# Optimization experiments

Measured on AMD Instinct MI355X. Metric: run time of the kernel, lower is better.

The kernel has to match this reference:

```python
import jax, jax.numpy as jnp
import numpy as np

N = 50000
E = 800000
EPS = 1e-5


def setup_inputs() -> dict:
    key = jax.random.key(0)
    ks = jax.random.split(key, 12)

    def w(k, fi, fo):
        return jax.random.normal(k, (fi, fo), dtype=jnp.float32) * (1.0 / np.sqrt(fi))

    return {
        "x": jax.random.normal(ks[0], (N, 128), dtype=jnp.float32),
        "edge_index": jax.random.randint(ks[1], (2, E), 0, N, dtype=jnp.int32),
        "W1": w(ks[2], 128, 256), "b1": jnp.zeros((256,), jnp.float32),
        "g1": jnp.ones((256,), jnp.float32), "be1": jnp.zeros((256,), jnp.float32),
        "W2": w(ks[3], 256, 128), "b2": jnp.zeros((128,), jnp.float32),
        "g2": jnp.ones((128,), jnp.float32), "be2": jnp.zeros((128,), jnp.float32),
        "W3": w(ks[4], 128, 64), "b3": jnp.zeros((64,), jnp.float32),
        "g3": jnp.ones((64,), jnp.float32), "be3": jnp.zeros((64,), jnp.float32),
        "W4": w(ks[5], 64, 40), "b4": jnp.zeros((40,), jnp.float32),
        "a": jnp.array(0.25, dtype=jnp.float32),  # PReLU single shared weight
    }


def _gcn_norm(edge_index, n):
    # PyG GCNConv default: add self-loops, symmetric normalization.
    loop = jnp.arange(n, dtype=edge_index.dtype)
    s = jnp.concatenate([edge_index[0], loop])  # [E+N] source nodes
    d = jnp.concatenate([edge_index[1], loop])  # [E+N] dest nodes
    deg = jax.ops.segment_sum(jnp.ones_like(s, dtype=jnp.float32), d, num_segments=n)
    dinv = jax.lax.rsqrt(jnp.maximum(deg, 1.0))  # deg >= 1 due to self-loops
    norm = dinv[s] * dinv[d]                     # [E+N]
    return s, d, norm


def _gcn_conv(x, W, b, s, d, norm, n):
    xw = x @ W                                   # [N, F_out] dense transform
    msg = xw[s] * norm[:, None]                  # gather + edge scaling
    return jax.ops.segment_sum(msg, d, num_segments=n) + b  # scatter-add


def _bn(x, g, b):
    # BatchNorm over nodes (training statistics, biased variance)
    m = jnp.mean(x, axis=0)
    v = jnp.var(x, axis=0)
    return (x - m) * jax.lax.rsqrt(v + EPS) * g + b


def _prelu(x, a):
    return jnp.where(x >= 0, x, a * x)


def reference(x, edge_index, W1, b1, g1, be1, W2, b2, g2, be2,
              W3, b3, g3, be3, W4, b4, a):
    n = x.shape[0]
    s, d, norm = _gcn_norm(edge_index, n)
    h = _prelu(_bn(_gcn_conv(x, W1, b1, s, d, norm, n), g1, be1), a)
    h = _prelu(_bn(_gcn_conv(h, W2, b2, s, d, norm, n), g2, be2), a)
    h = _prelu(_bn(_gcn_conv(h, W3, b3, s, d, norm, n), g3, be3), a)
    h = _gcn_conv(h, W4, b4, s, d, norm, n)
    return jax.nn.log_softmax(h, axis=1)
```

## Files before the change

kernel.cpp:

```cpp
#include <hip/hip_runtime.h>
#include <cstdint>
#include <cmath>

typedef _Float16 half_t;
typedef _Float16 h2 __attribute__((ext_vector_type(2)));
typedef _Float16 h8 __attribute__((ext_vector_type(8)));
typedef float f4 __attribute__((ext_vector_type(4)));


__global__ __launch_bounds__(256) void csr_hist_kernel(const int* __restrict__ ei_dst,
                                                       int* __restrict__ hcnt,
                                                       int E, int B, int NB, int chunk) {
    __shared__ int hist[256];
    int t = threadIdx.x;
    hist[t] = 0;
    __syncthreads();
    int base = blockIdx.x * chunk;
    int lim = min(base + chunk, E);
    for (int e = base + t; e < lim; e += 256) {
        int dst = ei_dst[e];
        atomicAdd(&hist[dst >> 8], 1);
    }
    __syncthreads();
    if (t < B) hcnt[t * NB + blockIdx.x] = hist[t];
}

__global__ __launch_bounds__(256) void csr_bscan_kernel(int* __restrict__ hcnt,
                                                        int* __restrict__ btot, int NB) {
    __shared__ int sh[256];
    int b = blockIdx.x, t = threadIdx.x;
    int v = (t < NB) ? hcnt[b * NB + t] : 0;
    sh[t] = v;
    __syncthreads();
    for (int off = 1; off < 256; off <<= 1) {
        int u = (t >= off) ? sh[t - off] : 0;
        __syncthreads();
        sh[t] += u;
        __syncthreads();
    }
    if (t < NB) hcnt[b * NB + t] = sh[t] - v;
    if (t == 255) btot[b] = sh[255];
}

__global__ __launch_bounds__(256) void csr_ebase_kernel(const int* __restrict__ btot,
                                                        int* __restrict__ edge_base,
                                                        int* __restrict__ row_ptr,
                                                        int B, int E, int n) {
    __shared__ int sh[256];
    int t = threadIdx.x;
    int v = (t < B) ? btot[t] : 0;
    sh[t] = v;
    __syncthreads();
    for (int off = 1; off < 256; off <<= 1) {
        int u = (t >= off) ? sh[t - off] : 0;
        __syncthreads();
        sh[t] += u;
        __syncthreads();
    }
    if (t < B) edge_base[t] = sh[t] - v;
    if (t == 0) {
        edge_base[B] = E;
        row_ptr[n] = E;
    }
}

__global__ __launch_bounds__(256) void csr_part_kernel(const int* __restrict__ ei,
                                                       const int* __restrict__ hcnt,
                                                       const int* __restrict__ edge_base,
                                                       unsigned int* __restrict__ ebuf,
                                                       int E, int B, int NB, int chunk) {
    __shared__ int lcur[256];
    int t = threadIdx.x;
    if (t < B) lcur[t] = edge_base[t] + hcnt[t * NB + blockIdx.x];
    __syncthreads();
    int base = blockIdx.x * chunk;
    int lim = min(base + chunk, E);
    for (int e = base + t; e < lim; e += 256) {
        int src = ei[e];
        int dst = ei[E + e];
        int b = dst >> 8;
        int pos = atomicAdd(&lcur[b], 1);
        ebuf[pos] = ((unsigned int)(dst & 255) << 16) | (unsigned int)src;
    }
}

__global__ __launch_bounds__(256) void csr_fill_kernel(const unsigned int* __restrict__ ebuf,
                                                       const int* __restrict__ edge_base,
                                                       int* __restrict__ row_ptr,
                                                       float* __restrict__ dinv,
                                                       unsigned short* __restrict__ colidx,
                                                       int n) {
    __shared__ int cnt[256];
    __shared__ int sc[256];
    __shared__ int cur[256];
    int b = blockIdx.x;
    int t = threadIdx.x;
    int seg_beg = edge_base[b];
    int seg_end = edge_base[b + 1];
    cnt[t] = 0;
    __syncthreads();
    for (int e = seg_beg + t; e < seg_end; e += 256)
        atomicAdd(&cnt[ebuf[e] >> 16], 1);
    __syncthreads();
    sc[t] = cnt[t];
    __syncthreads();
    for (int off = 1; off < 256; off <<= 1) {
        int u = (t >= off) ? sc[t - off] : 0;
        __syncthreads();
        sc[t] += u;
        __syncthreads();
    }
    int excl = seg_beg + sc[t] - cnt[t];
    int node = (b << 8) + t;
    if (node < n) {
        row_ptr[node] = excl;
        dinv[node] = rsqrtf((float)cnt[t] + 1.0f);
    }
    cur[t] = excl;
    __syncthreads();
    for (int e = seg_beg + t; e < seg_end; e += 256) {
        unsigned int p = ebuf[e];
        int pos = atomicAdd(&cur[p >> 16], 1);
        colidx[pos] = (unsigned short)(p & 0xffff);
    }
}


__global__ void f2h_kernel(const float* __restrict__ x, half_t* __restrict__ xh, int total4) {
    int i = blockIdx.x * blockDim.x + threadIdx.x;
    if (i < total4) {
        float4 v = *(const float4*)&x[i * 4];
        half_t* p = xh + (size_t)i * 4;
        p[0] = (half_t)v.x; p[1] = (half_t)v.y; p[2] = (half_t)v.z; p[3] = (half_t)v.w;
    }
}

__global__ __launch_bounds__(256) void wtall_kernel(const float* __restrict__ W1,
                                                    const float* __restrict__ W2,
                                                    const float* __restrict__ W3,
                                                    const float* __restrict__ W4,
                                                    half_t* __restrict__ W1t,
                                                    half_t* __restrict__ W2t,
                                                    half_t* __restrict__ W3t,
                                                    half_t* __restrict__ W4t) {
    int idx = blockIdx.x * blockDim.x + threadIdx.x;
    if (idx < 32768) {
        int n = idx >> 7, k = idx & 127;
        W1t[idx] = (half_t)W1[k * 256 + n];
    } else if (idx < 65536) {
        int r = idx - 32768;
        int n = r >> 8, k = r & 255;
        W2t[r] = (half_t)W2[k * 128 + n];
    } else if (idx < 73728) {
        int r = idx - 65536;
        int n = r >> 7, k = r & 127;
        W3t[r] = (half_t)W3[k * 64 + n];
    } else if (idx < 77824) {
        int r = idx - 73728;
        int n = r >> 6, k = r & 63;
        W4t[r] = (n < 40) ? (half_t)W4[k * 40 + n] : (half_t)0.f;
    }
}


__global__ __launch_bounds__(256) void aggh128_kernel(const half_t* __restrict__ in,
                                                      half_t* __restrict__ out,
                                                      const int* __restrict__ row_ptr,
                                                      const unsigned short* __restrict__ colidx,
                                                      const float* __restrict__ dinv, int n) {
    int node = blockIdx.x * 4 + (threadIdx.x >> 6);
    if (node >= n) return;
    int c = threadIdx.x & 63;
    float dv = dinv[node];
    h2 self = *(const h2*)(in + (size_t)node * 128 + 2 * c);
    float acc0 = dv * (float)self[0], acc1 = dv * (float)self[1];
    int beg = row_ptr[node], end = row_ptr[node + 1];
    for (int k = beg; k < end; k += 8) {
        int idx[8]; float w[8]; h2 v[8];
#pragma unroll
        for (int j = 0; j < 8; ++j) idx[j] = colidx[k + j];
#pragma unroll
        for (int j = 0; j < 8; ++j) w[j] = (k + j < end) ? dinv[idx[j]] : 0.f;
#pragma unroll
        for (int j = 0; j < 8; ++j) v[j] = *(const h2*)(in + (size_t)idx[j] * 128 + 2 * c);
#pragma unroll
        for (int j = 0; j < 8; ++j) {
            acc0 = fmaf(w[j], (float)v[j][0], acc0);
            acc1 = fmaf(w[j], (float)v[j][1], acc1);
        }
    }
    h2 r;
    r[0] = (half_t)(dv * acc0);
    r[1] = (half_t)(dv * acc1);
    *(h2*)(out + (size_t)node * 128 + 2 * c) = r;
}

__global__ __launch_bounds__(256) void aggh64_kernel(const half_t* __restrict__ in,
                                                     half_t* __restrict__ out,
                                                     const int* __restrict__ row_ptr,
                                                     const unsigned short* __restrict__ colidx,
                                                     const float* __restrict__ dinv, int n) {
    int node = blockIdx.x * 4 + (threadIdx.x >> 6);
    if (node >= n) return;
    int c = threadIdx.x & 63;
    float dv = dinv[node];
    float acc = dv * (float)in[(size_t)node * 64 + c];
    int beg = row_ptr[node], end = row_ptr[node + 1];
    for (int k = beg; k < end; k += 8) {
        int idx[8]; float w[8]; float v[8];
#pragma unroll
        for (int j = 0; j < 8; ++j) idx[j] = colidx[k + j];
#pragma unroll
        for (int j = 0; j < 8; ++j) w[j] = (k + j < end) ? dinv[idx[j]] : 0.f;
#pragma unroll
        for (int j = 0; j < 8; ++j) v[j] = (float)in[(size_t)idx[j] * 64 + c];
#pragma unroll
        for (int j = 0; j < 8; ++j) acc = fmaf(w[j], v[j], acc);
    }
    out[(size_t)node * 64 + c] = (half_t)(dv * acc);
}

__global__ __launch_bounds__(256) void aggsm64_kernel(const half_t* __restrict__ in,
                                                      float* __restrict__ out,
                                                      const int* __restrict__ row_ptr,
                                                      const unsigned short* __restrict__ colidx,
                                                      const float* __restrict__ dinv,
                                                      const float* __restrict__ b4, int n) {
    int node = blockIdx.x * 4 + (threadIdx.x >> 6);
    if (node >= n) return;
    int c = threadIdx.x & 31;
    float dv = dinv[node];
    h2 self = *(const h2*)(in + (size_t)node * 64 + 2 * c);
    float acc0 = dv * (float)self[0], acc1 = dv * (float)self[1];
    int beg = row_ptr[node], end = row_ptr[node + 1];
    for (int k = beg; k < end; k += 8) {
        int idx[8]; float w[8]; h2 v[8];
#pragma unroll
        for (int j = 0; j < 8; ++j) idx[j] = colidx[k + j];
#pragma unroll
        for (int j = 0; j < 8; ++j) w[j] = (k + j < end) ? dinv[idx[j]] : 0.f;
#pragma unroll
        for (int j = 0; j < 8; ++j) v[j] = *(const h2*)(in + (size_t)idx[j] * 64 + 2 * c);
#pragma unroll
        for (int j = 0; j < 8; ++j) {
            acc0 = fmaf(w[j], (float)v[j][0], acc0);
            acc1 = fmaf(w[j], (float)v[j][1], acc1);
        }
    }
    int col0 = 2 * c, col1 = 2 * c + 1;
    float z0 = (col0 < 40) ? (dv * acc0 + b4[col0]) : -INFINITY;
    float z1 = (col1 < 40) ? (dv * acc1 + b4[col1]) : -INFINITY;
    float m = fmaxf(z0, z1);
#pragma unroll
    for (int off = 16; off > 0; off >>= 1) m = fmaxf(m, __shfl_xor(m, off, 64));
    float e0 = (col0 < 40) ? expf(z0 - m) : 0.f;
    float e1 = (col1 < 40) ? expf(z1 - m) : 0.f;
    float s = e0 + e1;
#pragma unroll
    for (int off = 16; off > 0; off >>= 1) s += __shfl_xor(s, off, 64);
    float ls = logf(s);
    if (c < 20) {
        float2 r = make_float2(z0 - m - ls, z1 - m - ls);
        *(float2*)(out + (size_t)node * 40 + 2 * c) = r;
    }
}


template <int K, int NT, bool FUSE>
__global__ __launch_bounds__(256) void mgemm_kernel(const half_t* __restrict__ A,
                                                    const half_t* __restrict__ Wt,
                                                    const float* __restrict__ AB,
                                                    const float* __restrict__ pa,
                                                    half_t* __restrict__ C,
                                                    int M, int Nc, int nTiles) {
    constexpr int NR = NT * 16;
    constexpr int CH = K / 8;
    constexpr int LOG_CH = (CH == 8) ? 3 : (CH == 16 ? 4 : 5);
    __shared__ half_t wlds[NR * K];

    for (int idx = threadIdx.x; idx < NR * CH; idx += 256) {
        int row = idx >> LOG_CH;
        int c = idx & (CH - 1);
        *(h8*)(wlds + ((size_t)c * NR + row) * 8) = *(const h8*)(Wt + (size_t)idx * 8);
    }
    int wave = threadIdx.x >> 6;
    int lane = threadIdx.x & 63;
    int l16 = lane & 15, kgrp = lane >> 4;
    float alpha = FUSE ? pa[0] : 0.f;
    __syncthreads();

    for (int tile = blockIdx.x; tile < nTiles; tile += gridDim.x) {
        int r0 = tile * 64 + wave * 16;
        int arow = r0 + l16;
        bool rowok = (arow < M);
        const half_t* Ap = A + (size_t)arow * K + kgrp * 8;
        h8 af[K / 32];
#pragma unroll
        for (int kk = 0; kk < K / 32; ++kk) {
            h8 v;
            if (rowok) {
                v = *(const h8*)(Ap + kk * 32);
            } else {
#pragma unroll
                for (int j = 0; j < 8; ++j) v[j] = (half_t)0.f;
            }
            if (FUSE) {
                int kb = kk * 32 + kgrp * 8;
#pragma unroll
                for (int j = 0; j < 8; ++j) {
                    float u = (float)v[j] * AB[kb + j] + AB[256 + kb + j];
                    u = (u >= 0.f) ? u : alpha * u;
                    v[j] = (half_t)u;
                }
            }
            af[kk] = v;
        }

        for (int nt = 0; nt < NT; ++nt) {
            f4 acc = {0.f, 0.f, 0.f, 0.f};
#pragma unroll
            for (int kk = 0; kk < K / 32; ++kk) {
                h8 bf = *(const h8*)(wlds + ((size_t)(kk * 4 + kgrp) * NR + nt * 16 + l16) * 8);
                acc = __builtin_amdgcn_mfma_f32_16x16x32_f16(af[kk], bf, acc, 0, 0, 0);
            }
            int col = nt * 16 + l16;
            if (col < Nc) {
#pragma unroll
                for (int j = 0; j < 4; ++j) {
                    int row = r0 + kgrp * 4 + j;
                    if (row < M) C[(size_t)row * Nc + col] = (half_t)acc[j];
                }
            }
        }
    }
}


template <int F>
__global__ __launch_bounds__(256) void stats2_kernel(const half_t* __restrict__ z,
                                                     float* __restrict__ sums, int n) {
    constexpr int CB = F / 8;
    constexpr int RG = 256 / CB;
    __shared__ float red[256][16];
    int t = threadIdx.x;
    int cb = t % CB;
    int rg = t / CB;
    float sm[8], sq[8];
#pragma unroll
    for (int j = 0; j < 8; ++j) { sm[j] = 0.f; sq[j] = 0.f; }
    for (int r = blockIdx.x * RG + rg; r < n; r += gridDim.x * RG) {
        h8 v = *(const h8*)(z + (size_t)r * F + cb * 8);
#pragma unroll
        for (int j = 0; j < 8; ++j) {
            float f = (float)v[j];
            sm[j] += f;
            sq[j] = fmaf(f, f, sq[j]);
        }
    }
#pragma unroll
    for (int j = 0; j < 8; ++j) { red[t][j] = sm[j]; red[t][8 + j] = sq[j]; }
    __syncthreads();
    for (int o = t; o < 2 * F; o += 256) {
        int c = o % F, kind = o / F;
        int cbo = c >> 3, ci = (c & 7) + kind * 8;
        float v = 0.f;
#pragma unroll
        for (int g = 0; g < RG; ++g) v += red[g * CB + cbo][ci];
        atomicAdd(&sums[kind * 256 + c], v);
    }
}

__global__ void bnfin_kernel(const float* __restrict__ sums, const float* __restrict__ g,
                             const float* __restrict__ be, float* __restrict__ AB, int n, int F) {
    int c = threadIdx.x;
    if (c >= F) return;
    float mean = sums[c] / (float)n;
    float var = sums[256 + c] / (float)n - mean * mean;
    float rstd = rsqrtf(var + 1e-5f);
    float sc = g[c] * rstd;
    AB[c] = sc;
    AB[256 + c] = be[c] - mean * sc;
}


extern "C" void kernel_launch(void* const* d_in, const int* in_sizes, int n_in,
                              void* d_out, int out_size, void* d_ws, size_t ws_size,
                              hipStream_t stream) {
    const float* x   = (const float*)d_in[0];
    const int*   ei  = (const int*)d_in[1];
    const float* W1  = (const float*)d_in[2];
    const float* g1  = (const float*)d_in[4];
    const float* be1 = (const float*)d_in[5];
    const float* W2  = (const float*)d_in[6];
    const float* g2  = (const float*)d_in[8];
    const float* be2 = (const float*)d_in[9];
    const float* W3  = (const float*)d_in[10];
    const float* g3  = (const float*)d_in[12];
    const float* be3 = (const float*)d_in[13];
    const float* W4  = (const float*)d_in[14];
    const float* b4  = (const float*)d_in[15];
    const float* pa  = (const float*)d_in[16];

    int N = in_sizes[0] / 128;
    int E = in_sizes[1] / 2;
    int B = (N + 255) >> 8;
    int chunk = (((E + 255) / 256) + 255) & ~255;
    int NB = (E + chunk - 1) / chunk;

    char* ws = (char*)d_ws;
    size_t off = 0;
    auto carve = [&](size_t bytes) -> char* {
        char* p = ws + off;
        off += (bytes + 255) & ~(size_t)255;
        return p;
    };
    float*          dinv      = (float*)carve((size_t)N * 4);
    int*            row_ptr   = (int*)carve((size_t)(N + 1) * 4);
    int*            hcnt      = (int*)carve((size_t)B * NB * 4);
    int*            btot      = (int*)carve((size_t)B * 4);
    int*            edge_base = (int*)carve((size_t)(B + 1) * 4);
    unsigned int*   ebuf      = (unsigned int*)carve((size_t)E * 4);
    unsigned short* colidx    = (unsigned short*)carve((size_t)(E + 16) * 2);
    float*          stats     = (float*)carve(3 * 512 * 4);
    float*          bnAB      = (float*)carve(512 * 4);
    half_t* W1t = (half_t*)carve((size_t)256 * 128 * 2);
    half_t* W2t = (half_t*)carve((size_t)128 * 256 * 2);
    half_t* W3t = (half_t*)carve((size_t)64 * 128 * 2);
    half_t* W4t = (half_t*)carve((size_t)64 * 64 * 2);
    half_t* hA  = (half_t*)carve((size_t)N * 256 * 2);
    half_t* hB  = (half_t*)carve((size_t)N * 128 * 2);
    half_t* hC  = (half_t*)carve((size_t)N * 128 * 2);
    half_t* hD1 = (half_t*)carve((size_t)N * 64 * 2);
    half_t* hD2 = (half_t*)carve((size_t)N * 64 * 2);
    half_t* hE  = (half_t*)carve((size_t)N * 64 * 2);
    (void)n_in; (void)out_size; (void)ws_size;

    hipMemsetAsync(colidx + E, 0, 32, stream);
    hipMemsetAsync(stats, 0, 3 * 512 * 4, stream);

    csr_hist_kernel<<<NB, 256, 0, stream>>>(ei + E, hcnt, E, B, NB, chunk);
    csr_bscan_kernel<<<B, 256, 0, stream>>>(hcnt, btot, NB);
    csr_ebase_kernel<<<1, 256, 0, stream>>>(btot, edge_base, row_ptr, B, E, N);
    csr_part_kernel<<<NB, 256, 0, stream>>>(ei, hcnt, edge_base, ebuf, E, B, NB, chunk);
    csr_fill_kernel<<<B, 256, 0, stream>>>(ebuf, edge_base, row_ptr, dinv, colidx, N);

    wtall_kernel<<<(77824 + 255) / 256, 256, 0, stream>>>(W1, W2, W3, W4, W1t, W2t, W3t, W4t);

    int nTiles = (N + 63) / 64;
    int gb = nTiles < 512 ? nTiles : 512;
    int ab = (N + 3) / 4;

    f2h_kernel<<<(N * 128 / 4 + 255) / 256, 256, 0, stream>>>(x, hB, N * 128 / 4);
    aggh128_kernel<<<ab, 256, 0, stream>>>(hB, hC, row_ptr, colidx, dinv, N);
    mgemm_kernel<128, 16, false><<<gb, 256, 0, stream>>>(hC, W1t, nullptr, nullptr, hA,
                                                         N, 256, nTiles);
    stats2_kernel<256><<<512, 256, 0, stream>>>(hA, stats, N);
    bnfin_kernel<<<1, 256, 0, stream>>>(stats, g1, be1, bnAB, N, 256);

    mgemm_kernel<256, 8, true><<<gb, 256, 0, stream>>>(hA, W2t, bnAB, pa, hB, N, 128, nTiles);
    aggh128_kernel<<<ab, 256, 0, stream>>>(hB, hC, row_ptr, colidx, dinv, N);
    stats2_kernel<128><<<512, 256, 0, stream>>>(hC, stats + 512, N);
    bnfin_kernel<<<1, 256, 0, stream>>>(stats + 512, g2, be2, bnAB, N, 128);

    mgemm_kernel<128, 4, true><<<gb, 256, 0, stream>>>(hC, W3t, bnAB, pa, hD1, N, 64, nTiles);
    aggh64_kernel<<<ab, 256, 0, stream>>>(hD1, hD2, row_ptr, colidx, dinv, N);
    stats2_kernel<64><<<512, 256, 0, stream>>>(hD2, stats + 1024, N);
    bnfin_kernel<<<1, 256, 0, stream>>>(stats + 1024, g3, be3, bnAB, N, 64);

    mgemm_kernel<64, 4, true><<<gb, 256, 0, stream>>>(hD2, W4t, bnAB, pa, hE, N, 64, nTiles);
    aggsm64_kernel<<<ab, 256, 0, stream>>>(hE, (float*)d_out, row_ptr, colidx, dinv, b4, N);
}
```

Before: 298.2 us.

## Fuse BatchNorm statistics into GEMM/aggregation epilogues and drop conversion kernels

BatchNorm sum and sum-of-squares accumulation moves into the epilogues of the GEMM and aggregation kernels, using shared-memory atomics followed by global atomics. The BN scale/offset finalize is recomputed in each consuming GEMM's prologue. The first-layer aggregation now reads fp32 input directly, removing the separate f2h conversion pass. The two memsets are merged into one. This removes six kernel launches and the extra full-tensor reads done by stats2, at the cost of more shared-memory atomic contention in the aggregation and GEMM kernels.

```diff
diff --git a/kernel.cpp b/kernel.cpp
--- a/kernel.cpp
+++ b/kernel.cpp
@@ -125,15 +125,6 @@
     }
 }
 
-
-__global__ void f2h_kernel(const float* __restrict__ x, half_t* __restrict__ xh, int total4) {
-    int i = blockIdx.x * blockDim.x + threadIdx.x;
-    if (i < total4) {
-        float4 v = *(const float4*)&x[i * 4];
-        half_t* p = xh + (size_t)i * 4;
-        p[0] = (half_t)v.x; p[1] = (half_t)v.y; p[2] = (half_t)v.z; p[3] = (half_t)v.w;
-    }
-}
 
 __global__ __launch_bounds__(256) void wtall_kernel(const float* __restrict__ W1,
                                                     const float* __restrict__ W2,
@@ -163,7 +154,7 @@
 }
 
 
-__global__ __launch_bounds__(256) void aggh128_kernel(const half_t* __restrict__ in,
+__global__ __launch_bounds__(256) void agg128f_kernel(const float* __restrict__ in,
                                                       half_t* __restrict__ out,
                                                       const int* __restrict__ row_ptr,
                                                       const unsigned short* __restrict__ colidx,
@@ -172,21 +163,21 @@
     if (node >= n) return;
     int c = threadIdx.x & 63;
     float dv = dinv[node];
-    h2 self = *(const h2*)(in + (size_t)node * 128 + 2 * c);
-    float acc0 = dv * (float)self[0], acc1 = dv * (float)self[1];
+    float2 self = *(const float2*)(in + (size_t)node * 128 + 2 * c);
+    float acc0 = dv * self.x, acc1 = dv * self.y;
     int beg = row_ptr[node], end = row_ptr[node + 1];
     for (int k = beg; k < end; k += 8) {
-        int idx[8]; float w[8]; h2 v[8];
+        int idx[8]; float w[8]; float2 v[8];
 #pragma unroll
         for (int j = 0; j < 8; ++j) idx[j] = colidx[k + j];
 #pragma unroll
         for (int j = 0; j < 8; ++j) w[j] = (k + j < end) ? dinv[idx[j]] : 0.f;
 #pragma unroll
-        for (int j = 0; j < 8; ++j) v[j] = *(const h2*)(in + (size_t)idx[j] * 128 + 2 * c);
+        for (int j = 0; j < 8; ++j) v[j] = *(const float2*)(in + (size_t)idx[j] * 128 + 2 * c);
 #pragma unroll
         for (int j = 0; j < 8; ++j) {
-            acc0 = fmaf(w[j], (float)v[j][0], acc0);
-            acc1 = fmaf(w[j], (float)v[j][1], acc1);
+            acc0 = fmaf(w[j], v[j].x, acc0);
+            acc1 = fmaf(w[j], v[j].y, acc1);
         }
     }
     h2 r;
@@ -195,29 +186,110 @@
     *(h2*)(out + (size_t)node * 128 + 2 * c) = r;
 }
 
+template <bool STATS>
+__global__ __launch_bounds__(256) void aggh128_kernel(const half_t* __restrict__ in,
+                                                      half_t* __restrict__ out,
+                                                      const int* __restrict__ row_ptr,
+                                                      const unsigned short* __restrict__ colidx,
+                                                      const float* __restrict__ dinv,
+                                                      float* __restrict__ sout, int n) {
+    __shared__ float ssum[128], ssq[128];
+    int t = threadIdx.x;
+    if (STATS) {
+        if (t < 128) { ssum[t] = 0.f; ssq[t] = 0.f; }
+        __syncthreads();
+    }
+    int node = blockIdx.x * 4 + (t >> 6);
+    bool active = node < n;
+    int c = t & 63;
+    float dv = 0.f, acc0 = 0.f, acc1 = 0.f;
+    if (active) {
+        dv = dinv[node];
+        h2 self = *(const h2*)(in + (size_t)node * 128 + 2 * c);
+        acc0 = dv * (float)self[0];
+        acc1 = dv * (float)self[1];
+        int beg = row_ptr[node], end = row_ptr[node + 1];
+        for (int k = beg; k < end; k += 8) {
+            int idx[8]; float w[8]; h2 v[8];
+#pragma unroll
+            for (int j = 0; j < 8; ++j) idx[j] = colidx[k + j];
+#pragma unroll
+            for (int j = 0; j < 8; ++j) w[j] = (k + j < end) ? dinv[idx[j]] : 0.f;
+#pragma unroll
+            for (int j = 0; j < 8; ++j) v[j] = *(const h2*)(in + (size_t)idx[j] * 128 + 2 * c);
+#pragma unroll
+            for (int j = 0; j < 8; ++j) {
+                acc0 = fmaf(w[j], (float)v[j][0], acc0);
+                acc1 = fmaf(w[j], (float)v[j][1], acc1);
+            }
+        }
+        float v0 = dv * acc0, v1 = dv * acc1;
+        h2 r;
+        r[0] = (half_t)v0;
+        r[1] = (half_t)v1;
+        *(h2*)(out + (size_t)node * 128 + 2 * c) = r;
+        if (STATS) {
+            atomicAdd(&ssum[2 * c], v0);
+            atomicAdd(&ssq[2 * c], v0 * v0);
+            atomicAdd(&ssum[2 * c + 1], v1);
+            atomicAdd(&ssq[2 * c + 1], v1 * v1);
+        }
+    }
+    if (STATS) {
+        __syncthreads();
+        if (t < 128) {
+            atomicAdd(&sout[t], ssum[t]);
+            atomicAdd(&sout[256 + t], ssq[t]);
+        }
+    }
+}
+
+template <bool STATS>
 __global__ __launch_bounds__(256) void aggh64_kernel(const half_t* __restrict__ in,
                                                      half_t* __restrict__ out,
                                                      const int* __restrict__ row_ptr,
                                                      const unsigned short* __restrict__ colidx,
-                                                     const float* __restrict__ dinv, int n) {
-    int node = blockIdx.x * 4 + (threadIdx.x >> 6);
-    if (node >= n) return;
-    int c = threadIdx.x & 63;
-    float dv = dinv[node];
-    float acc = dv * (float)in[(size_t)node * 64 + c];
-    int beg = row_ptr[node], end = row_ptr[node + 1];
-    for (int k = beg; k < end; k += 8) {
-        int idx[8]; float w[8]; float v[8];
-#pragma unroll
-        for (int j = 0; j < 8; ++j) idx[j] = colidx[k + j];
-#pragma unroll
-        for (int j = 0; j < 8; ++j) w[j] = (k + j < end) ? dinv[idx[j]] : 0.f;
-#pragma unroll
-        for (int j = 0; j < 8; ++j) v[j] = (float)in[(size_t)idx[j] * 64 + c];
-#pragma unroll
-        for (int j = 0; j < 8; ++j) acc = fmaf(w[j], v[j], acc);
-    }
-    out[(size_t)node * 64 + c] = (half_t)(dv * acc);
+                                                     const float* __restrict__ dinv,
+                                                     float* __restrict__ sout, int n) {
+    __shared__ float ssum[64], ssq[64];
+    int t = threadIdx.x;
+    if (STATS) {
+        if (t < 64) { ssum[t] = 0.f; ssq[t] = 0.f; }
+        __syncthreads();
+    }
+    int node = blockIdx.x * 4 + (t >> 6);
+    bool active = node < n;
+    int c = t & 63;
+    float dv = 0.f, acc = 0.f;
+    if (active) {
+        dv = dinv[node];
+        acc = dv * (float)in[(size_t)node * 64 + c];
+        int beg = row_ptr[node], end = row_ptr[node + 1];
+        for (int k = beg; k < end; k += 8) {
+            int idx[8]; float w[8]; float v[8];
+#pragma unroll
+            for (int j = 0; j < 8; ++j) idx[j] = colidx[k + j];
+#pragma unroll
+            for (int j = 0; j < 8; ++j) w[j] = (k + j < end) ? dinv[idx[j]] : 0.f;
+#pragma unroll
+            for (int j = 0; j < 8; ++j) v[j] = (float)in[(size_t)idx[j] * 64 + c];
+#pragma unroll
+            for (int j = 0; j < 8; ++j) acc = fmaf(w[j], v[j], acc);
+        }
+        float vv = dv * acc;
+        out[(size_t)node * 64 + c] = (half_t)vv;
+        if (STATS) {
+            atomicAdd(&ssum[c], vv);
+            atomicAdd(&ssq[c], vv * vv);
+        }
+    }
+    if (STATS) {
+        __syncthreads();
+        if (t < 64) {
+            atomicAdd(&sout[t], ssum[t]);
+            atomicAdd(&sout[256 + t], ssq[t]);
+        }
+    }
 }
 
 __global__ __launch_bounds__(256) void aggsm64_kernel(const half_t* __restrict__ in,
@@ -266,28 +338,50 @@
 }
 
 
-template <int K, int NT, bool FUSE>
+template <int K, int NT, bool BNC, bool STATS>
 __global__ __launch_bounds__(256) void mgemm_kernel(const half_t* __restrict__ A,
                                                     const half_t* __restrict__ Wt,
-                                                    const float* __restrict__ AB,
+                                                    const float* __restrict__ bn_stats,
+                                                    const float* __restrict__ g,
+                                                    const float* __restrict__ be,
                                                     const float* __restrict__ pa,
+                                                    float* __restrict__ stats_out,
                                                     half_t* __restrict__ C,
                                                     int M, int Nc, int nTiles) {
     constexpr int NR = NT * 16;
     constexpr int CH = K / 8;
     constexpr int LOG_CH = (CH == 8) ? 3 : (CH == 16 ? 4 : 5);
     __shared__ half_t wlds[NR * K];
-
-    for (int idx = threadIdx.x; idx < NR * CH; idx += 256) {
+    __shared__ float sc_l[K], of_l[K];
+    __shared__ float ssum[NR > 64 ? NR : 64], ssq[NR > 64 ? NR : 64];
+
+    int t = threadIdx.x;
+    for (int idx = t; idx < NR * CH; idx += 256) {
         int row = idx >> LOG_CH;
         int c = idx & (CH - 1);
         *(h8*)(wlds + ((size_t)c * NR + row) * 8) = *(const h8*)(Wt + (size_t)idx * 8);
     }
-    int wave = threadIdx.x >> 6;
-    int lane = threadIdx.x & 63;
+    if (BNC && t < K) {
+        float inv_n = 1.0f / (float)M;
+        float mean = bn_stats[t] * inv_n;
+        float var = bn_stats[256 + t] * inv_n - mean * mean;
+        float rstd = rsqrtf(var + 1e-5f);
+        float s = g[t] * rstd;
+        sc_l[t] = s;
+        of_l[t] = be[t] - mean * s;
+    }
+    if (STATS && t < NR) { ssum[t] = 0.f; ssq[t] = 0.f; }
+    int wave = t >> 6;
+    int lane = t & 63;
     int l16 = lane & 15, kgrp = lane >> 4;
-    float alpha = FUSE ? pa[0] : 0.f;
-    __syncthreads();
+    float alpha = BNC ? pa[0] : 0.f;
+    __syncthreads();
+
+    float psum[NT], psq[NT];
+    if (STATS) {
+#pragma unroll
+        for (int nt = 0; nt < NT; ++nt) { psum[nt] = 0.f; psq[nt] = 0.f; }
+    }
 
     for (int tile = blockIdx.x; tile < nTiles; tile += gridDim.x) {
         int r0 = tile * 64 + wave * 16;
@@ -304,11 +398,11 @@
 #pragma unroll
                 for (int j = 0; j < 8; ++j) v[j] = (half_t)0.f;
             }
-            if (FUSE) {
+            if (BNC) {
                 int kb = kk * 32 + kgrp * 8;
 #pragma unroll
                 for (int j = 0; j < 8; ++j) {
-                    float u = (float)v[j] * AB[kb + j] + AB[256 + kb + j];
+                    float u = (float)v[j] * sc_l[kb + j] + of_l[kb + j];
                     u = (u >= 0.f) ? u : alpha * u;
                     v[j] = (half_t)u;
                 }
@@ -328,58 +422,30 @@
 #pragma unroll
                 for (int j = 0; j < 4; ++j) {
                     int row = r0 + kgrp * 4 + j;
-                    if (row < M) C[(size_t)row * Nc + col] = (half_t)acc[j];
+                    if (row < M) {
+                        C[(size_t)row * Nc + col] = (half_t)acc[j];
+                        if (STATS) {
+                            psum[nt] += acc[j];
+                            psq[nt] = fmaf(acc[j], acc[j], psq[nt]);
+                        }
+                    }
                 }
             }
         }
     }
-}
-
-
-template <int F>
-__global__ __launch_bounds__(256) void stats2_kernel(const half_t* __restrict__ z,
-                                                     float* __restrict__ sums, int n) {
-    constexpr int CB = F / 8;
-    constexpr int RG = 256 / CB;
-    __shared__ float red[256][16];
-    int t = threadIdx.x;
-    int cb = t % CB;
-    int rg = t / CB;
-    float sm[8], sq[8];
-#pragma unroll
-    for (int j = 0; j < 8; ++j) { sm[j] = 0.f; sq[j] = 0.f; }
-    for (int r = blockIdx.x * RG + rg; r < n; r += gridDim.x * RG) {
-        h8 v = *(const h8*)(z + (size_t)r * F + cb * 8);
-#pragma unroll
-        for (int j = 0; j < 8; ++j) {
-            float f = (float)v[j];
-            sm[j] += f;
-            sq[j] = fmaf(f, f, sq[j]);
-        }
-    }
-#pragma unroll
-    for (int j = 0; j < 8; ++j) { red[t][j] = sm[j]; red[t][8 + j] = sq[j]; }
-    __syncthreads();
-    for (int o = t; o < 2 * F; o += 256) {
-        int c = o % F, kind = o / F;
-        int cbo = c >> 3, ci = (c & 7) + kind * 8;
-        float v = 0.f;
-#pragma unroll
-        for (int g = 0; g < RG; ++g) v += red[g * CB + cbo][ci];
-        atomicAdd(&sums[kind * 256 + c], v);
-    }
-}
-
-__global__ void bnfin_kernel(const float* __restrict__ sums, const float* __restrict__ g,
-                             const float* __restrict__ be, float* __restrict__ AB, int n, int F) {
-    int c = threadIdx.x;
-    if (c >= F) return;
-    float mean = sums[c] / (float)n;
-    float var = sums[256 + c] / (float)n - mean * mean;
-    float rstd = rsqrtf(var + 1e-5f);
-    float sc = g[c] * rstd;
-    AB[c] = sc;
-    AB[256 + c] = be[c] - mean * sc;
+
+    if (STATS) {
+#pragma unroll
+        for (int nt = 0; nt < NT; ++nt) {
+            atomicAdd(&ssum[nt * 16 + l16], psum[nt]);
+            atomicAdd(&ssq[nt * 16 + l16], psq[nt]);
+        }
+        __syncthreads();
+        if (t < NR) {
+            atomicAdd(&stats_out[t], ssum[t]);
+            atomicAdd(&stats_out[256 + t], ssq[t]);
+        }
+    }
 }
 
 
@@ -422,7 +488,6 @@
     unsigned int*   ebuf      = (unsigned int*)carve((size_t)E * 4);
     unsigned short* colidx    = (unsigned short*)carve((size_t)(E + 16) * 2);
     float*          stats     = (float*)carve(3 * 512 * 4);
-    float*          bnAB      = (float*)carve(512 * 4);
     half_t* W1t = (half_t*)carve((size_t)256 * 128 * 2);
     half_t* W2t = (half_t*)carve((size_t)128 * 256 * 2);
     half_t* W3t = (half_t*)carve((size_t)64 * 128 * 2);
@@ -435,8 +500,11 @@
     half_t* hE  = (half_t*)carve((size_t)N * 64 * 2);
     (void)n_in; (void)out_size; (void)ws_size;
 
-    hipMemsetAsync(colidx + E, 0, 32, stream);
-    hipMemsetAsync(stats, 0, 3 * 512 * 4, stream);
+    {
+        char* z0 = (char*)(colidx + E);
+        char* z1 = (char*)stats + 3 * 512 * 4;
+        hipMemsetAsync(z0, 0, (size_t)(z1 - z0), stream);
+    }
 
     csr_hist_kernel<<<NB, 256, 0, stream>>>(ei + E, hcnt, E, B, NB, chunk);
     csr_bscan_kernel<<<B, 256, 0, stream>>>(hcnt, btot, NB);
@@ -450,23 +518,21 @@
     int gb = nTiles < 512 ? nTiles : 512;
     int ab = (N + 3) / 4;
 
-    f2h_kernel<<<(N * 128 / 4 + 255) / 256, 256, 0, stream>>>(x, hB, N * 128 / 4);
-    aggh128_kernel<<<ab, 256, 0, stream>>>(hB, hC, row_ptr, colidx, dinv, N);
-    mgemm_kernel<128, 16, false><<<gb, 256, 0, stream>>>(hC, W1t, nullptr, nullptr, hA,
-                                                         N, 256, nTiles);
-    stats2_kernel<256><<<512, 256, 0, stream>>>(hA, stats, N);
-    bnfin_kernel<<<1, 256, 0, stream>>>(stats, g1, be1, bnAB, N, 256);
-
-    mgemm_kernel<256, 8, true><<<gb, 256, 0, stream>>>(hA, W2t, bnAB, pa, hB, N, 128, nTiles);
-    aggh128_kernel<<<ab, 256, 0, stream>>>(hB, hC, row_ptr, colidx, dinv, N);
-    stats2_kernel<128><<<512, 256, 0, stream>>>(hC, stats + 512, N);
-    bnfin_kernel<<<1, 256, 0, stream>>>(stats + 512, g2, be2, bnAB, N, 128);
-
-    mgemm_kernel<128, 4, true><<<gb, 256, 0, stream>>>(hC, W3t, bnAB, pa, hD1, N, 64, nTiles);
-    aggh64_kernel<<<ab, 256, 0, stream>>>(hD1, hD2, row_ptr, colidx, dinv, N);
-    stats2_kernel<64><<<512, 256, 0, stream>>>(hD2, stats + 1024, N);
-    bnfin_kernel<<<1, 256, 0, stream>>>(stats + 1024, g3, be3, bnAB, N, 64);
-
-    mgemm_kernel<64, 4, true><<<gb, 256, 0, stream>>>(hD2, W4t, bnAB, pa, hE, N, 64, nTiles);
+    agg128f_kernel<<<ab, 256, 0, stream>>>(x, hC, row_ptr, colidx, dinv, N);
+    mgemm_kernel<128, 16, false, true><<<gb, 256, 0, stream>>>(
+        hC, W1t, nullptr, nullptr, nullptr, nullptr, stats, hA, N, 256, nTiles);
+
+    mgemm_kernel<256, 8, true, false><<<gb, 256, 0, stream>>>(
+        hA, W2t, stats, g1, be1, pa, nullptr, hB, N, 128, nTiles);
+    aggh128_kernel<true><<<ab, 256, 0, stream>>>(hB, hC, row_ptr, colidx, dinv,
+                                                 stats + 512, N);
+
+    mgemm_kernel<128, 4, true, false><<<gb, 256, 0, stream>>>(
+        hC, W3t, stats + 512, g2, be2, pa, nullptr, hD1, N, 64, nTiles);
+    aggh64_kernel<true><<<ab, 256, 0, stream>>>(hD1, hD2, row_ptr, colidx, dinv,
+                                                stats + 1024, N);
+
+    mgemm_kernel<64, 4, true, false><<<gb, 256, 0, stream>>>(
+        hD2, W4t, stats + 1024, g3, be3, pa, nullptr, hE, N, 64, nTiles);
     aggsm64_kernel<<<ab, 256, 0, stream>>>(hE, (float*)d_out, row_ptr, colidx, dinv, b4, N);
 }
```

Measured after the change: 857.4 us. 188% more time.
